# Performance work log

Measured on AMD Instinct MI355X. Metric: run time of the kernel, lower is better.

The kernel has to match this reference:

```python
import jax, jax.numpy as jnp
import numpy as np


def setup_inputs() -> dict:
    key = jax.random.key(0)
    k1, k2 = jax.random.split(key)
    x = jax.random.normal(k1, (4, 4096, 128), dtype=jnp.float32)
    kernel = jax.random.normal(k2, (3, 128, 64), dtype=jnp.float32)
    return {"x": x, "kernel": kernel}


def reference(x, kernel):
    # QKV projections: x [B,N,Din] @ kernel[i] [Din,Dout] -> [B,N,Dout]
    WQ = jnp.einsum('bnd,de->bne', x, kernel[0])
    WK = jnp.einsum('bnd,de->bne', x, kernel[1])
    WV = jnp.einsum('bnd,de->bne', x, kernel[2])
    d_out = WV.shape[-1]
    # scaled dot-product scores [B,N,N]
    scores = jnp.einsum('bqe,bke->bqk', WQ, WK) / jnp.sqrt(jnp.float32(d_out))
    attn = jax.nn.softmax(scores, axis=-1)
    return jnp.einsum('bqk,bke->bqe', attn, WV)
```

## Files before the change

kernel.cpp:

```cpp
#include <hip/hip_runtime.h>


typedef __attribute__((ext_vector_type(8))) short bf16x8;
typedef __attribute__((ext_vector_type(16))) float f32x16;
typedef __attribute__((ext_vector_type(4))) unsigned u32x4;
typedef unsigned short us;

__device__ __forceinline__ us f2bf(float f) {
  unsigned u = __builtin_bit_cast(unsigned, f);
  u += 0x7FFFu + ((u >> 16) & 1u);
  return (us)(u >> 16);
}
__device__ __forceinline__ float bf2f(us h) {
  unsigned u = ((unsigned)h) << 16;
  return __builtin_bit_cast(float, u);
}
__device__ __forceinline__ float hi_part(float v) {
  return __builtin_bit_cast(float,
         __builtin_bit_cast(unsigned, v) & 0xFFFF0000u);
}
__device__ __forceinline__ f32x16 mfma(bf16x8 a, bf16x8 b, f32x16 c) {
  return __builtin_amdgcn_mfma_f32_32x32x16_bf16(a, b, c, 0, 0, 0);
}
__device__ __forceinline__ unsigned pk2t(float a, float b) {
  return __builtin_amdgcn_perm(__builtin_bit_cast(unsigned, b),
                               __builtin_bit_cast(unsigned, a), 0x07060302u);
}
__device__ __forceinline__ void dma16(const us* g, us* l) {
  __builtin_amdgcn_global_load_lds(
      (const __attribute__((address_space(1))) unsigned*)g,
      (__attribute__((address_space(3))) unsigned*)l, 16, 0, 0);
}
#define EXP2(x) __builtin_amdgcn_exp2f(x)

#define NSEG 8
#define ITERS 8

__global__ __launch_bounds__(384, 1) void qkv_kernel(
    const float* __restrict__ x, const float* __restrict__ w,
    us* __restrict__ Qhi, us* __restrict__ Qlo,
    us* __restrict__ Kbh, us* __restrict__ Kbl, us* __restrict__ Vb)
{
  __shared__ unsigned ttile[32 * 193];
  const int t = threadIdx.x;
  const int rb = blockIdx.x;
  const int wid = t >> 6, lane = t & 63;
  const int l31 = lane & 31, h = lane >> 5;
  const int rbase = rb * 32;
  const float* xrow = x + (size_t)(rbase + l31) * 128;

  bf16x8 wbh[8], wbl[8];
  {
    const float sc = (wid < 2) ? 0.18033688011112042f : 1.0f;
    const float* wp = w + (wid >> 1) * 8192 + (wid & 1) * 32 + l31 + h * 512;
    #pragma unroll
    for (int ks = 0; ks < 8; ++ks) {
      u32x4 hv, lv;
      #pragma unroll
      for (int jp = 0; jp < 4; ++jp) {
        const float va = wp[(ks * 16 + 2 * jp) * 64] * sc;
        const float vb = wp[(ks * 16 + 2 * jp + 1) * 64] * sc;
        hv[jp] = pk2t(va, vb);
        lv[jp] = pk2t(va - hi_part(va), vb - hi_part(vb));
      }
      wbh[ks] = __builtin_bit_cast(bf16x8, hv);
      wbl[ks] = __builtin_bit_cast(bf16x8, lv);
    }
  }

  f32x16 acc = {};
  #pragma unroll
  for (int ks = 0; ks < 8; ++ks) {
    const int d0 = ks * 16 + h * 8;
    const float4 xa = *(const float4*)(xrow + d0);
    const float4 xb = *(const float4*)(xrow + d0 + 4);
    const float xv[8] = {xa.x, xa.y, xa.z, xa.w, xb.x, xb.y, xb.z, xb.w};
    u32x4 ahv, alv;
    #pragma unroll
    for (int jp = 0; jp < 4; ++jp) {
      const float va = xv[2 * jp], vb = xv[2 * jp + 1];
      ahv[jp] = pk2t(va, vb);
      alv[jp] = pk2t(va - hi_part(va), vb - hi_part(vb));
    }
    const bf16x8 ah = __builtin_bit_cast(bf16x8, ahv);
    const bf16x8 al = __builtin_bit_cast(bf16x8, alv);
    acc = mfma(ah, wbh[ks], acc);
    acc = mfma(al, wbh[ks], acc);
    acc = mfma(ah, wbl[ks], acc);
  }

  const bool isV = (wid >= 4);
  #pragma unroll
  for (int r = 0; r < 16; ++r) {
    const int rl = (r & 3) + 8 * (r >> 2) + 4 * h;
    const float v = acc[r];
    const unsigned e = isV ? (unsigned)f2bf(v)
                           : pk2t(v, v - hi_part(v));
    ttile[rl * 193 + wid * 32 + l31] = e;
  }
  __syncthreads();

  if (t < 64) {
    const int row = t >> 1, cb = (t & 1) * 32;
    const int grow = rbase + row;
    unsigned hw[16], lw[16];
    #pragma unroll
    for (int j = 0; j < 16; ++j) {
      unsigned a = ttile[row * 193 + cb + 2 * j];
      unsigned bv = ttile[row * 193 + cb + 2 * j + 1];
      hw[j] = (a & 0xffffu) | (bv << 16);
      lw[j] = (a >> 16) | (bv & 0xffff0000u);
    }
    #pragma unroll
    for (int j = 0; j < 4; ++j) {
      uint4 hv = {hw[4 * j], hw[4 * j + 1], hw[4 * j + 2], hw[4 * j + 3]};
      uint4 lv = {lw[4 * j], lw[4 * j + 1], lw[4 * j + 2], lw[4 * j + 3]};
      *(uint4*)(Qhi + (size_t)grow * 64 + cb + 8 * j) = hv;
      *(uint4*)(Qlo + (size_t)grow * 64 + cb + 8 * j) = lv;
    }
  } else if (t < 192) {
    const int bb = rbase >> 12;
    const int kt = (rbase & 4095) >> 6;
    const int m = (rbase >> 5) & 1;
    const size_t kbb = (size_t)bb * 262144 + (size_t)kt * 4096 + m * 256;
    #pragma unroll
    for (int i2 = 0; i2 < 2; ++i2) {
      const int c = (t - 64) + 128 * i2;
      const int r = c & 31, hh = (c >> 5) & 1, ks = c >> 6;
      unsigned hw[4], lw[4];
      #pragma unroll
      for (int j = 0; j < 4; ++j) {
        unsigned a = ttile[r * 193 + 64 + 16 * ks + 8 * hh + 2 * j];
        unsigned bv = ttile[r * 193 + 64 + 16 * ks + 8 * hh + 2 * j + 1];
        hw[j] = (a & 0xffffu) | (bv << 16);
        lw[j] = (a >> 16) | (bv & 0xffff0000u);
      }
      const size_t off = kbb + (size_t)(ks * 4 + 2 * hh) * 256 + r * 8;
      uint4 hv = {hw[0], hw[1], hw[2], hw[3]};
      uint4 lv = {lw[0], lw[1], lw[2], lw[3]};
      *(uint4*)(Kbh + off) = hv;
      *(uint4*)(Kbl + off) = lv;
    }
  } else if (t < 320) {
    const int bb = rbase >> 12;
    const int nb = rbase & 4095;
    #pragma unroll
    for (int i2 = 0; i2 < 2; ++i2) {
      const int c = (t - 192) + 128 * i2;
      const int e = c >> 2, nc = c & 3;
      unsigned p[4];
      #pragma unroll
      for (int j = 0; j < 4; ++j) {
        unsigned a = ttile[(nc * 8 + 2 * j) * 193 + 128 + e];
        unsigned bv = ttile[(nc * 8 + 2 * j + 1) * 193 + 128 + e];
        p[j] = (a & 0xffffu) | (bv << 16);
      }
      uint4 pv = {p[0], p[1], p[2], p[3]};
      const int n0 = nb + nc * 8;
      const int kt = n0 >> 6, sub = n0 & 63;
      const int ks = sub >> 4, hh = (sub >> 3) & 1;
      const int dt = e >> 5, lv = e & 31;
      *(uint4*)(Vb + (size_t)bb * 262144 +
                ((((kt * 4 + ks) * 2 + hh) * 2 + dt) * 256 + lv * 8)) = pv;
    }
  }
}

__global__ __launch_bounds__(256, 3) void attn_kernel(
    const us* __restrict__ Qhi, const us* __restrict__ Qlo,
    const us* __restrict__ Kbh, const us* __restrict__ Kbl,
    const us* __restrict__ Vb,
    us* __restrict__ Opart, float* __restrict__ Mpart,
    float* __restrict__ Lpart)
{
  __shared__ us stage[2][12288];
  __shared__ float alds[4][32];

  const int bx = blockIdx.x;
  const int xc = bx & 7, b = xc >> 1;
  const int idx = ((bx >> 3) << 1) | (xc & 1);
  const int seg = idx & (NSEG - 1), qg = idx >> 3;
  const int t = threadIdx.x;
  const int wid = t >> 6, lane = t & 63;
  const int l31 = lane & 31, h = lane >> 5;
  const int q0 = qg * 128 + wid * 32;
  const int u = (b * 4096 + q0) >> 5;
  const size_t pb = (size_t)u * NSEG + seg;

  bf16x8 qh[4], ql[4];
  {
    const size_t rg = (size_t)(b * 4096 + q0 + l31) * 64;
    #pragma unroll
    for (int ks = 0; ks < 4; ++ks) {
      qh[ks] = *(const bf16x8*)(Qhi + rg + ks * 16 + h * 8);
      ql[ks] = *(const bf16x8*)(Qlo + rg + ks * 16 + h * 8);
    }
  }
  const size_t kbase = (size_t)b * 262144;

  {
    const size_t kb0 = kbase + (size_t)(seg * ITERS) * 4096;
    #pragma unroll
    for (int i = 0; i < 6; ++i) {
      const int c = wid * 6 + i;
      const us* src = (c < 8)  ? Kbh + kb0 + c * 512
                    : (c < 16) ? Kbl + kb0 + (c - 8) * 512
                               : Vb  + kb0 + (c - 16) * 512;
      dma16(src + lane * 8, &stage[0][c * 512]);
    }
  }
  __syncthreads();

  f32x16 o[2] = {};
  float mrun = -__builtin_inff();
  float lrun = 0.f;

  for (int it = 0; it < ITERS; ++it) {
    const int cur = it & 1;
    const us* sb = &stage[cur][0];

    if (it + 1 < ITERS) {
      const size_t kbn = kbase + (size_t)(seg * ITERS + it + 1) * 4096;
      #pragma unroll
      for (int i = 0; i < 6; ++i) {
        const int c = wid * 6 + i;
        const us* src = (c < 8)  ? Kbh + kbn + c * 512
                      : (c < 16) ? Kbl + kbn + (c - 8) * 512
                                 : Vb  + kbn + (c - 16) * 512;
        dma16(src + lane * 8, &stage[cur ^ 1][c * 512]);
      }
    }

    f32x16 s[2] = {};
    __builtin_amdgcn_s_setprio(1);
    #pragma unroll
    for (int ks = 0; ks < 4; ++ks) {
      #pragma unroll
      for (int m = 0; m < 2; ++m) {
        const int ko = (ks * 4 + 2 * h + m) * 256 + l31 * 8;
        const bf16x8 ah = *(const bf16x8*)(sb + ko);
        const bf16x8 al = *(const bf16x8*)(sb + 4096 + ko);
        s[m] = mfma(ah, qh[ks], s[m]);
        s[m] = mfma(al, qh[ks], s[m]);
        s[m] = mfma(ah, ql[ks], s[m]);
      }
    }
    __builtin_amdgcn_s_setprio(0);

    float va = fmaxf(s[0][0], s[1][0]);
    float vb = fmaxf(s[0][1], s[1][1]);
    #pragma unroll
    for (int r = 2; r < 16; r += 2) {
      va = fmaxf(va, fmaxf(s[0][r], s[1][r]));
      vb = fmaxf(vb, fmaxf(s[0][r + 1], s[1][r + 1]));
    }
    float vm = fmaxf(va, vb);
    vm = fmaxf(vm, __shfl_xor(vm, 32));

    if (!__all(vm <= mrun - 24.f)) {
      const float mnew = (vm > mrun + 0.5f) ? vm : mrun;
      const float alpha = EXP2(mrun - mnew);
      float sm0 = 0.f, sm1 = 0.f;
      unsigned pp[2][8];
      #pragma unroll
      for (int m = 0; m < 2; ++m) {
        #pragma unroll
        for (int p = 0; p < 8; ++p) {
          const float p0 = EXP2(s[m][2 * p] - mnew);
          const float p1 = EXP2(s[m][2 * p + 1] - mnew);
          sm0 += p0;
          sm1 += p1;
          pp[m][p] = pk2t(p0, p1);
        }
      }
      float sum = sm0 + sm1;
      sum += __shfl_xor(sum, 32);
      lrun = lrun * alpha + sum;
      mrun = mnew;

      if (__any(alpha != 1.f)) {
        if (!h) alds[wid][l31] = alpha;
        #pragma unroll
        for (int g = 0; g < 4; ++g) {
          const float4 af4 = *(const float4*)(&alds[wid][8 * g + 4 * h]);
          #pragma unroll
          for (int rr = 0; rr < 4; ++rr) {
            const int r = 4 * g + rr;
            const float a = (rr == 0) ? af4.x : (rr == 1) ? af4.y
                           : (rr == 2) ? af4.z : af4.w;
            o[0][r] *= a;
            o[1][r] *= a;
          }
        }
      }

      __builtin_amdgcn_s_setprio(1);
      #pragma unroll
      for (int ks = 0; ks < 4; ++ks) {
        const int vo = 8192 + (ks * 4 + 2 * h) * 256 + l31 * 8;
        const bf16x8 vf0 = *(const bf16x8*)(sb + vo);
        const bf16x8 vf1 = *(const bf16x8*)(sb + vo + 256);
        const int m = ks >> 1, base = 4 * (ks & 1);
        unsigned wx = pp[m][base + 0], wz = pp[m][base + 2];
        unsigned wy = pp[m][base + 1], ww = pp[m][base + 3];
        asm("v_permlane32_swap_b32 %0, %1" : "+v"(wx), "+v"(wz));
        asm("v_permlane32_swap_b32 %0, %1" : "+v"(wy), "+v"(ww));
        u32x4 wv;
        wv.x = wx;
        wv.y = wy;
        wv.z = wz;
        wv.w = ww;
        const bf16x8 af = __builtin_bit_cast(bf16x8, wv);
        o[0] = mfma(af, vf0, o[0]);
        o[1] = mfma(af, vf1, o[1]);
      }
      __builtin_amdgcn_s_setprio(0);
    }

    __syncthreads();
  }

  float* fw = ((float*)&stage[0][0]) + wid * (32 * 34);
  #pragma unroll
  for (int dt = 0; dt < 2; ++dt) {
    #pragma unroll
    for (int r = 0; r < 16; ++r) {
      const int qrow = (r & 3) + 8 * (r >> 2) + 4 * h;
      fw[qrow * 34 + l31] = o[dt][r];
    }
    #pragma unroll
    for (int jj = 0; jj < 2; ++jj) {
      const int chunk = lane + 64 * jj;
      const int rw = chunk >> 2, part = chunk & 3;
      const float* src = &fw[rw * 34 + part * 8];
      float2 a0 = *(const float2*)(src + 0);
      float2 a1 = *(const float2*)(src + 2);
      float2 a2 = *(const float2*)(src + 4);
      float2 a3 = *(const float2*)(src + 6);
      uint4 pkv;
      pkv.x = pk2t(a0.x, a0.y);
      pkv.y = pk2t(a1.x, a1.y);
      pkv.z = pk2t(a2.x, a2.y);
      pkv.w = pk2t(a3.x, a3.y);
      *(uint4*)(Opart + pb * 2048 + (size_t)rw * 64 + dt * 32 + part * 8) =
          pkv;
    }
  }
  if (!h) {
    Mpart[pb * 32 + l31] = mrun;
    Lpart[pb * 32 + l31] = lrun;
  }
}

__global__ __launch_bounds__(256, 1) void merge_kernel(
    const us* __restrict__ Opart, const float* __restrict__ Mpart,
    const float* __restrict__ Lpart, float* __restrict__ out)
{
  const int tg = blockIdx.x * 256 + threadIdx.x;
  const int q = tg >> 3, dc = (tg & 7) * 8;
  const int u = q >> 5, ql = q & 31;
  const int base = u * NSEG;
  float M = -__builtin_inff();
  #pragma unroll
  for (int s = 0; s < NSEG; ++s)
    M = fmaxf(M, Mpart[(size_t)(base + s) * 32 + ql]);
  float acc[8] = {};
  float den = 0.f;
  #pragma unroll
  for (int s = 0; s < NSEG; ++s) {
    const float wgt = EXP2(Mpart[(size_t)(base + s) * 32 + ql] - M);
    den += wgt * Lpart[(size_t)(base + s) * 32 + ql];
    const uint4 r = *(const uint4*)(Opart + (size_t)(base + s) * 2048 +
                                    ql * 64 + dc);
    const unsigned rw[4] = {r.x, r.y, r.z, r.w};
    #pragma unroll
    for (int j = 0; j < 4; ++j) {
      acc[2 * j]     += wgt * bf2f((us)(rw[j] & 0xffffu));
      acc[2 * j + 1] += wgt * bf2f((us)(rw[j] >> 16));
    }
  }
  const float inv = 1.f / den;
  float4 r0 = {acc[0] * inv, acc[1] * inv, acc[2] * inv, acc[3] * inv};
  float4 r1 = {acc[4] * inv, acc[5] * inv, acc[6] * inv, acc[7] * inv};
  *(float4*)(out + (size_t)q * 64 + dc) = r0;
  *(float4*)(out + (size_t)q * 64 + dc + 4) = r1;
}

extern "C" void kernel_launch(void* const* d_in, const int* in_sizes, int n_in,
                              void* d_out, int out_size, void* d_ws,
                              size_t ws_size, hipStream_t stream)
{
  const float* x = (const float*)d_in[0];
  const float* w = (const float*)d_in[1];
  float* out = (float*)d_out;
  char* ws = (char*)d_ws;

  const size_t T = 2097152;
  us* Qhi = (us*)(ws + 0 * T);
  us* Qlo = (us*)(ws + 1 * T);
  us* Kbh = (us*)(ws + 2 * T);
  us* Kbl = (us*)(ws + 3 * T);
  us* Vb  = (us*)(ws + 4 * T);
  char* pbase = ws + 5 * T;
  us* Opart = (us*)pbase;
  float* Mpart = (float*)(pbase + 16777216);
  float* Lpart = (float*)(pbase + 16777216 + 524288);

  hipLaunchKernelGGL(qkv_kernel, dim3(512), dim3(384), 0, stream,
                     x, w, Qhi, Qlo, Kbh, Kbl, Vb);
  hipLaunchKernelGGL(attn_kernel, dim3(1024), dim3(256), 0, stream,
                     Qhi, Qlo, Kbh, Kbl, Vb, Opart, Mpart, Lpart);
  hipLaunchKernelGGL(merge_kernel, dim3(512), dim3(256), 0, stream,
                     Opart, Mpart, Lpart, out);
}
```

Measured before the change: 118.2 us.

## Split softmax per 32-key half, read V directly from global, raise occupancy

```diff
diff --git a/kernel.cpp b/kernel.cpp
--- a/kernel.cpp
+++ b/kernel.cpp
@@ -166,14 +166,14 @@
   }
 }
 
-__global__ __launch_bounds__(256, 3) void attn_kernel(
+__global__ __launch_bounds__(256, 4) void attn_kernel(
     const us* __restrict__ Qhi, const us* __restrict__ Qlo,
     const us* __restrict__ Kbh, const us* __restrict__ Kbl,
     const us* __restrict__ Vb,
     us* __restrict__ Opart, float* __restrict__ Mpart,
     float* __restrict__ Lpart)
 {
-  __shared__ us stage[2][12288];
+  __shared__ us stage[2][8192];
   __shared__ float alds[4][32];
 
   const int bx = blockIdx.x;
@@ -201,11 +201,10 @@
   {
     const size_t kb0 = kbase + (size_t)(seg * ITERS) * 4096;
     #pragma unroll
-    for (int i = 0; i < 6; ++i) {
-      const int c = wid * 6 + i;
-      const us* src = (c < 8)  ? Kbh + kb0 + c * 512
-                    : (c < 16) ? Kbl + kb0 + (c - 8) * 512
-                               : Vb  + kb0 + (c - 16) * 512;
+    for (int i = 0; i < 4; ++i) {
+      const int c = wid * 4 + i;
+      const us* src = (c < 8) ? Kbh + kb0 + c * 512
+                              : Kbl + kb0 + (c - 8) * 512;
       dma16(src + lane * 8, &stage[0][c * 512]);
     }
   }
@@ -218,103 +217,102 @@
   for (int it = 0; it < ITERS; ++it) {
     const int cur = it & 1;
     const us* sb = &stage[cur][0];
+    const int KT = seg * ITERS + it;
 
     if (it + 1 < ITERS) {
-      const size_t kbn = kbase + (size_t)(seg * ITERS + it + 1) * 4096;
-      #pragma unroll
-      for (int i = 0; i < 6; ++i) {
-        const int c = wid * 6 + i;
-        const us* src = (c < 8)  ? Kbh + kbn + c * 512
-                      : (c < 16) ? Kbl + kbn + (c - 8) * 512
-                                 : Vb  + kbn + (c - 16) * 512;
+      const size_t kbn = kbase + (size_t)(KT + 1) * 4096;
+      #pragma unroll
+      for (int i = 0; i < 4; ++i) {
+        const int c = wid * 4 + i;
+        const us* src = (c < 8) ? Kbh + kbn + c * 512
+                                : Kbl + kbn + (c - 8) * 512;
         dma16(src + lane * 8, &stage[cur ^ 1][c * 512]);
       }
     }
 
-    f32x16 s[2] = {};
-    __builtin_amdgcn_s_setprio(1);
-    #pragma unroll
-    for (int ks = 0; ks < 4; ++ks) {
-      #pragma unroll
-      for (int m = 0; m < 2; ++m) {
+    #pragma unroll
+    for (int m = 0; m < 2; ++m) {
+      f32x16 s = {};
+      __builtin_amdgcn_s_setprio(1);
+      #pragma unroll
+      for (int ks = 0; ks < 4; ++ks) {
         const int ko = (ks * 4 + 2 * h + m) * 256 + l31 * 8;
         const bf16x8 ah = *(const bf16x8*)(sb + ko);
         const bf16x8 al = *(const bf16x8*)(sb + 4096 + ko);
-        s[m] = mfma(ah, qh[ks], s[m]);
-        s[m] = mfma(al, qh[ks], s[m]);
-        s[m] = mfma(ah, ql[ks], s[m]);
-      }
-    }
-    __builtin_amdgcn_s_setprio(0);
-
-    float va = fmaxf(s[0][0], s[1][0]);
-    float vb = fmaxf(s[0][1], s[1][1]);
-    #pragma unroll
-    for (int r = 2; r < 16; r += 2) {
-      va = fmaxf(va, fmaxf(s[0][r], s[1][r]));
-      vb = fmaxf(vb, fmaxf(s[0][r + 1], s[1][r + 1]));
-    }
-    float vm = fmaxf(va, vb);
-    vm = fmaxf(vm, __shfl_xor(vm, 32));
-
-    if (!__all(vm <= mrun - 24.f)) {
-      const float mnew = (vm > mrun + 0.5f) ? vm : mrun;
-      const float alpha = EXP2(mrun - mnew);
-      float sm0 = 0.f, sm1 = 0.f;
-      unsigned pp[2][8];
-      #pragma unroll
-      for (int m = 0; m < 2; ++m) {
+        s = mfma(ah, qh[ks], s);
+        s = mfma(al, qh[ks], s);
+        s = mfma(ah, ql[ks], s);
+      }
+      __builtin_amdgcn_s_setprio(0);
+
+      float va = fmaxf(s[0], s[1]);
+      float vb2 = fmaxf(s[2], s[3]);
+      #pragma unroll
+      for (int r = 4; r < 16; r += 2) {
+        va = fmaxf(va, s[r]);
+        vb2 = fmaxf(vb2, s[r + 1]);
+      }
+      float vm = fmaxf(va, vb2);
+      vm = fmaxf(vm, __shfl_xor(vm, 32));
+
+      if (!__all(vm <= mrun - 24.f)) {
+        const float mnew = (vm > mrun + 0.5f) ? vm : mrun;
+        const float alpha = EXP2(mrun - mnew);
+        float sm0 = 0.f, sm1 = 0.f;
+        unsigned pp[8];
         #pragma unroll
         for (int p = 0; p < 8; ++p) {
-          const float p0 = EXP2(s[m][2 * p] - mnew);
-          const float p1 = EXP2(s[m][2 * p + 1] - mnew);
+          const float p0 = EXP2(s[2 * p] - mnew);
+          const float p1 = EXP2(s[2 * p + 1] - mnew);
           sm0 += p0;
           sm1 += p1;
-          pp[m][p] = pk2t(p0, p1);
+          pp[p] = pk2t(p0, p1);
         }
-      }
-      float sum = sm0 + sm1;
-      sum += __shfl_xor(sum, 32);
-      lrun = lrun * alpha + sum;
-      mrun = mnew;
-
-      if (__any(alpha != 1.f)) {
-        if (!h) alds[wid][l31] = alpha;
-        #pragma unroll
-        for (int g = 0; g < 4; ++g) {
-          const float4 af4 = *(const float4*)(&alds[wid][8 * g + 4 * h]);
+        float sum = sm0 + sm1;
+        sum += __shfl_xor(sum, 32);
+        lrun = lrun * alpha + sum;
+        mrun = mnew;
+
+        if (__any(alpha != 1.f)) {
+          if (!h) alds[wid][l31] = alpha;
           #pragma unroll
-          for (int rr = 0; rr < 4; ++rr) {
-            const int r = 4 * g + rr;
-            const float a = (rr == 0) ? af4.x : (rr == 1) ? af4.y
-                           : (rr == 2) ? af4.z : af4.w;
-            o[0][r] *= a;
-            o[1][r] *= a;
+          for (int g = 0; g < 4; ++g) {
+            const float4 af4 = *(const float4*)(&alds[wid][8 * g + 4 * h]);
+            #pragma unroll
+            for (int rr = 0; rr < 4; ++rr) {
+              const int r = 4 * g + rr;
+              const float a = (rr == 0) ? af4.x : (rr == 1) ? af4.y
+                             : (rr == 2) ? af4.z : af4.w;
+              o[0][r] *= a;
+              o[1][r] *= a;
+            }
           }
         }
-      }
-
-      __builtin_amdgcn_s_setprio(1);
-      #pragma unroll
-      for (int ks = 0; ks < 4; ++ks) {
-        const int vo = 8192 + (ks * 4 + 2 * h) * 256 + l31 * 8;
-        const bf16x8 vf0 = *(const bf16x8*)(sb + vo);
-        const bf16x8 vf1 = *(const bf16x8*)(sb + vo + 256);
-        const int m = ks >> 1, base = 4 * (ks & 1);
-        unsigned wx = pp[m][base + 0], wz = pp[m][base + 2];
-        unsigned wy = pp[m][base + 1], ww = pp[m][base + 3];
-        asm("v_permlane32_swap_b32 %0, %1" : "+v"(wx), "+v"(wz));
-        asm("v_permlane32_swap_b32 %0, %1" : "+v"(wy), "+v"(ww));
-        u32x4 wv;
-        wv.x = wx;
-        wv.y = wy;
-        wv.z = wz;
-        wv.w = ww;
-        const bf16x8 af = __builtin_bit_cast(bf16x8, wv);
-        o[0] = mfma(af, vf0, o[0]);
-        o[1] = mfma(af, vf1, o[1]);
-      }
-      __builtin_amdgcn_s_setprio(0);
+
+        __builtin_amdgcn_s_setprio(1);
+        #pragma unroll
+        for (int ks2 = 0; ks2 < 2; ++ks2) {
+          const int ksg = 2 * m + ks2;
+          const size_t vo = kbase +
+              (size_t)(((KT * 4 + ksg) * 2 + h) * 2) * 256 + l31 * 8;
+          const bf16x8 vf0 = *(const bf16x8*)(Vb + vo);
+          const bf16x8 vf1 = *(const bf16x8*)(Vb + vo + 256);
+          const int base = 4 * ks2;
+          unsigned wx = pp[base + 0], wz = pp[base + 2];
+          unsigned wy = pp[base + 1], ww = pp[base + 3];
+          asm("v_permlane32_swap_b32 %0, %1" : "+v"(wx), "+v"(wz));
+          asm("v_permlane32_swap_b32 %0, %1" : "+v"(wy), "+v"(ww));
+          u32x4 wv;
+          wv.x = wx;
+          wv.y = wy;
+          wv.z = wz;
+          wv.w = ww;
+          const bf16x8 af = __builtin_bit_cast(bf16x8, wv);
+          o[0] = mfma(af, vf0, o[0]);
+          o[1] = mfma(af, vf1, o[1]);
+        }
+        __builtin_amdgcn_s_setprio(0);
+      }
     }
 
     __syncthreads();
```

New measurement: 118.2 us. Within noise of the previous version (+0.0%).
